# Kernel optimization log

Hardware: AMD Instinct MI355X
Metric: run time of the kernel (lower is better)

Reference implementation:

```python
import jax, jax.numpy as jnp
import numpy as np

N = 40000       # nodes
DEG = 16        # in-degree per node (self-constructed so in_deg > 0)
E = N * DEG     # edges
DIN = 128       # in_ent_feats == out_ent_feats
H = 8           # num_heads
D = DIN // H    # head_dim = 16
FF = 4 * DIN    # FFN hidden
HOPS = 5
ALPHA = 0.15
EPS = 1e-5


def _ln(x, g, b):
    m = jnp.mean(x, axis=-1, keepdims=True)
    v = jnp.mean((x - m) ** 2, axis=-1, keepdims=True)
    return (x - m) / jnp.sqrt(v + EPS) * g + b


def setup_inputs() -> dict:
    key = jax.random.key(0)
    ks = jax.random.split(key, 12)
    s = 0.05
    feat = jax.random.normal(ks[0], (N, DIN), dtype=jnp.float32)
    src = jax.random.randint(ks[1], (E,), 0, N, dtype=jnp.int32)
    # every node gets exactly DEG incoming edges -> in_degree > 0 everywhere
    dst = jnp.repeat(jnp.arange(N, dtype=jnp.int32), DEG)
    return {
        "feat": feat,
        "Wh": jax.random.normal(ks[2], (DIN, DIN), dtype=jnp.float32) * s,
        "Wt": jax.random.normal(ks[3], (DIN, DIN), dtype=jnp.float32) * s,
        "We": jax.random.normal(ks[4], (DIN, DIN), dtype=jnp.float32) * s,
        "attn_p": jax.random.normal(ks[5], (H, D), dtype=jnp.float32) * s,
        "g_head": jax.random.normal(ks[6], (H, D), dtype=jnp.float32) * s,
        "g_tail": jax.random.normal(ks[7], (H, D), dtype=jnp.float32) * s,
        "ln1_g": jnp.ones((DIN,), jnp.float32),
        "ln1_b": jnp.zeros((DIN,), jnp.float32),
        "ln2_g": jnp.ones((DIN,), jnp.float32),
        "ln2_b": jnp.zeros((DIN,), jnp.float32),
        "W1": jax.random.normal(ks[8], (FF, DIN), dtype=jnp.float32) * s,
        "b1": jnp.zeros((FF,), jnp.float32),
        "W2": jax.random.normal(ks[9], (DIN, FF), dtype=jnp.float32) * s,
        "b2": jnp.zeros((DIN,), jnp.float32),
        "src": src,
        "dst": dst,
    }


def reference(feat, Wh, Wt, We, attn_p, g_head, g_tail, ln1_g, ln1_b,
              ln2_g, ln2_b, W1, b1, W2, b2, src, dst):
    n = feat.shape[0]
    h = _ln(feat, ln1_g, ln1_b)                      # feat_drop is identity (eval)
    fh = (h @ Wh.T).reshape(n, H, D)                 # feat_head
    ft = (h @ Wt.T).reshape(n, H, D)                 # feat_tail
    fe = (h @ We.T).reshape(n, H, D)                 # feat_enti ('ft' in dgl)

    # attention logits: (u_mul_v . attn).sum(-1) / head_dim, scaled by log(in_deg) of dst
    e = jnp.sum(fh[src] * ft[dst] * attn_p, axis=-1) / D          # [E, H]
    in_deg = jax.ops.segment_sum(jnp.ones_like(dst, jnp.float32), dst, num_segments=n)
    log_in = jnp.log(in_deg)                                       # [N]
    e = e * log_in[dst][:, None]

    # gate scores
    gh = jnp.sum(fh * g_head, axis=-1)                             # [N, H]
    gt = jnp.sum(ft * g_tail, axis=-1)
    gate = jax.nn.sigmoid(gh[src] + gt[dst])                       # [E, H]

    # weighted edge softmax (per-dst stabilized, gated)
    mx = jax.ops.segment_max(e, dst, num_segments=n)               # [N, H]
    tag = jnp.exp(e - mx[dst]) * gate
    ssum = jax.ops.segment_sum(tag, dst, num_segments=n)
    a = tag / ssum[dst]                                            # [E, H]

    # PPR diffusion
    feat0 = fe
    f = feat0
    for _ in range(HOPS):
        msg = f[src] * a[..., None]                                # [E, H, D]
        agg = jax.ops.segment_sum(msg, dst, num_segments=n)
        f = (1.0 - ALPHA) * agg + ALPHA * feat0

    # residual (Identity since in == out), flatten, FFN block
    rst = (f + feat.reshape(n, H, D)).reshape(n, -1)               # [N, DIN]
    x = _ln(rst, ln2_g, ln2_b)
    ff = jax.nn.relu(x @ W1.T + b1) @ W2.T + b2
    return ff + rst
```

## Files before the change

kernel.cpp:

```cpp
#include <hip/hip_runtime.h>
#include <math.h>

#define N_NODES 40000
#define DEG 16
#define DIN 128
#define NH 8
#define DH 16
#define FFDIM 512
#define ALPHA 0.15f
#define LNEPS 1e-5f

typedef __attribute__((ext_vector_type(8))) short bf16x8;
typedef __attribute__((ext_vector_type(4))) float f32x4;
typedef __attribute__((ext_vector_type(4))) unsigned int u32x4;

__device__ inline unsigned int f2bf(float f) {
    unsigned int u = __float_as_uint(f);
    return (u + 0x7fffu + ((u >> 16) & 1u)) >> 16;
}
__device__ inline float bflo(unsigned u) { return __uint_as_float(u << 16); }
__device__ inline float bfhi(unsigned u) { return __uint_as_float(u & 0xffff0000u); }

__device__ inline float dot8(u32x4 uf, u32x4 ut, const float* __restrict__ ap) {
    float s = 0.f;
#pragma unroll
    for (int k = 0; k < 4; ++k) {
        s += bflo(uf[k]) * bflo(ut[k]) * ap[2 * k]
           + bfhi(uf[k]) * bfhi(ut[k]) * ap[2 * k + 1];
    }
    return s;
}
__device__ inline float dot8w(u32x4 u, const float* __restrict__ w) {
    float s = 0.f;
#pragma unroll
    for (int k = 0; k < 4; ++k) {
        s += bflo(u[k]) * w[2 * k] + bfhi(u[k]) * w[2 * k + 1];
    }
    return s;
}

__device__ inline float wave_sum64(float v) {
#pragma unroll
    for (int m = 32; m >= 1; m >>= 1) v += __shfl_xor(v, m, 64);
    return v;
}

__global__ void cvt_weights(const float* __restrict__ wh, const float* __restrict__ wt,
                            const float* __restrict__ we, const float* __restrict__ w1,
                            const float* __restrict__ w2,
                            short* __restrict__ owh, short* __restrict__ owt,
                            short* __restrict__ owe, short* __restrict__ ow1,
                            short* __restrict__ ow2) {
    int i = blockIdx.x * 256 + threadIdx.x;
    if (i < 16384)       owh[i]          = (short)f2bf(wh[i]);
    else if (i < 32768)  owt[i - 16384]  = (short)f2bf(wt[i - 16384]);
    else if (i < 49152)  owe[i - 32768]  = (short)f2bf(we[i - 32768]);
    else if (i < 114688) ow1[i - 49152]  = (short)f2bf(w1[i - 49152]);
    else if (i < 180224) ow2[i - 114688] = (short)f2bf(w2[i - 114688]);
}

__global__ void ln_kernel(const float* __restrict__ in, const float* __restrict__ g,
                          const float* __restrict__ b, short* __restrict__ out, int n) {
    int wid  = (blockIdx.x * blockDim.x + threadIdx.x) >> 6;
    int lane = threadIdx.x & 63;
    if (wid >= n) return;
    float2 v = *(const float2*)(in + (size_t)wid * DIN + lane * 2);
    float mean = wave_sum64(v.x + v.y) * (1.0f / DIN);
    float dx = v.x - mean, dy = v.y - mean;
    float var = wave_sum64(dx * dx + dy * dy) * (1.0f / DIN);
    float rstd = rsqrtf(var + LNEPS);
    float2 gg = *(const float2*)(g + lane * 2);
    float2 bb = *(const float2*)(b + lane * 2);
    float o0 = dx * rstd * gg.x + bb.x, o1 = dy * rstd * gg.y + bb.y;
    unsigned int pack = f2bf(o0) | (f2bf(o1) << 16);
    *(unsigned int*)(out + (size_t)wid * DIN + lane * 2) = pack;
}

__global__ void add_ln_kernel(const float* __restrict__ f, const float* __restrict__ feat,
                              const float* __restrict__ g, const float* __restrict__ b,
                              float* __restrict__ rst, short* __restrict__ x, int n) {
    int wid  = (blockIdx.x * blockDim.x + threadIdx.x) >> 6;
    int lane = threadIdx.x & 63;
    if (wid >= n) return;
    float2 va = *(const float2*)(f + (size_t)wid * DIN + lane * 2);
    float2 vb = *(const float2*)(feat + (size_t)wid * DIN + lane * 2);
    float2 r = { va.x + vb.x, va.y + vb.y };
    *(float2*)(rst + (size_t)wid * DIN + lane * 2) = r;
    float mean = wave_sum64(r.x + r.y) * (1.0f / DIN);
    float dx = r.x - mean, dy = r.y - mean;
    float var = wave_sum64(dx * dx + dy * dy) * (1.0f / DIN);
    float rstd = rsqrtf(var + LNEPS);
    float2 gg = *(const float2*)(g + lane * 2);
    float2 bb = *(const float2*)(b + lane * 2);
    float o0 = dx * rstd * gg.x + bb.x, o1 = dy * rstd * gg.y + bb.y;
    unsigned int pack = f2bf(o0) | (f2bf(o1) << 16);
    *(unsigned int*)(x + (size_t)wid * DIN + lane * 2) = pack;
}

__global__ __launch_bounds__(256) void mfma_gemm(
        const short* __restrict__ A, const short* __restrict__ B,
        int M, int N, int K,
        const float* __restrict__ bias, const float* __restrict__ res, int relu,
        float* __restrict__ Cf, short* __restrict__ Cb) {
    __shared__ __align__(16) short Al[64 * 64];
    __shared__ __align__(16) short Bl[128 * 64];
    const int t  = threadIdx.x;
    const int bm = blockIdx.x * 64;
    const int bn = blockIdx.y * 128;
    const int w = t >> 6, lane = t & 63;
    const int wr = w >> 1, wc = w & 1;
    const int l15 = lane & 15, l4 = lane >> 4;
    f32x4 acc[2][4] = {};
    for (int k0 = 0; k0 < K; k0 += 64) {
        __syncthreads();
#pragma unroll
        for (int q = 0; q < 2; ++q) {
            int c = t + q * 256;
            int r = c >> 3, kb = c & 7;
            bf16x8 v = *(const bf16x8*)(A + (size_t)(bm + r) * K + k0 + kb * 8);
            *(bf16x8*)(Al + (r * 8 + (kb ^ (r & 7))) * 8) = v;
        }
#pragma unroll
        for (int q = 0; q < 4; ++q) {
            int c = t + q * 256;
            int r = c >> 3, kb = c & 7;
            bf16x8 v = *(const bf16x8*)(B + (size_t)(bn + r) * K + k0 + kb * 8);
            *(bf16x8*)(Bl + (r * 8 + (kb ^ (r & 7))) * 8) = v;
        }
        __syncthreads();
#pragma unroll
        for (int kc = 0; kc < 2; ++kc) {
            bf16x8 af[2], bfr[4];
#pragma unroll
            for (int mf = 0; mf < 2; ++mf) {
                int row = wr * 32 + mf * 16 + l15;
                int kb = kc * 4 + l4;
                af[mf] = *(const bf16x8*)(Al + (row * 8 + (kb ^ (row & 7))) * 8);
            }
#pragma unroll
            for (int nf = 0; nf < 4; ++nf) {
                int row = wc * 64 + nf * 16 + l15;
                int kb = kc * 4 + l4;
                bfr[nf] = *(const bf16x8*)(Bl + (row * 8 + (kb ^ (row & 7))) * 8);
            }
#pragma unroll
            for (int mf = 0; mf < 2; ++mf)
#pragma unroll
                for (int nf = 0; nf < 4; ++nf)
                    acc[mf][nf] = __builtin_amdgcn_mfma_f32_16x16x32_bf16(
                        af[mf], bfr[nf], acc[mf][nf], 0, 0, 0);
        }
    }
#pragma unroll
    for (int mf = 0; mf < 2; ++mf) {
#pragma unroll
        for (int nf = 0; nf < 4; ++nf) {
            int gcol = bn + wc * 64 + nf * 16 + l15;
            float bv = bias ? bias[gcol] : 0.f;
#pragma unroll
            for (int r = 0; r < 4; ++r) {
                int grow = bm + wr * 32 + mf * 16 + l4 * 4 + r;
                float v = acc[mf][nf][r] + bv;
                if (relu) v = fmaxf(v, 0.f);
                size_t off = (size_t)grow * N + gcol;
                if (res) v += res[off];
                if (Cb) Cb[off] = (short)f2bf(v);
                if (Cf) Cf[off] = v;
            }
        }
    }
}

__global__ void attn_kernel(const short* __restrict__ fh, const short* __restrict__ ftl,
                            const float* __restrict__ g_head, const float* __restrict__ g_tail,
                            const float* __restrict__ attn_p, const int* __restrict__ src,
                            float* __restrict__ av, int n) {
    int wid  = (blockIdx.x * blockDim.x + threadIdx.x) >> 6;
    int lane = threadIdx.x & 63;
    if (wid >= n) return;
    int e  = lane & 15;
    int h0 = lane >> 4;
    int s = src[(size_t)wid * DEG + e];
    const short* fr0 = fh  + (size_t)s   * DIN + h0 * DH;
    const short* tr0 = ftl + (size_t)wid * DIN + h0 * DH;
    u32x4 f0a = *(const u32x4*)(fr0);
    u32x4 f0b = *(const u32x4*)(fr0 + 8);
    u32x4 t0a = *(const u32x4*)(tr0);
    u32x4 t0b = *(const u32x4*)(tr0 + 8);
    u32x4 f1a = *(const u32x4*)(fr0 + 64);
    u32x4 f1b = *(const u32x4*)(fr0 + 72);
    u32x4 t1a = *(const u32x4*)(tr0 + 64);
    u32x4 t1b = *(const u32x4*)(tr0 + 72);
    const float* ap0 = attn_p + h0 * DH;
    float v0 = dot8(f0a, t0a, ap0) + dot8(f0b, t0b, ap0 + 8);
    float v1 = dot8(f1a, t1a, ap0 + 64) + dot8(f1b, t1b, ap0 + 72);
    const float c = 0.17328679513998632f;
    v0 *= c; v1 *= c;
    const float* gh0 = g_head + h0 * DH;
    const float* gt0 = g_tail + h0 * DH;
    float gs0 = dot8w(f0a, gh0) + dot8w(f0b, gh0 + 8)
              + dot8w(t0a, gt0) + dot8w(t0b, gt0 + 8);
    float gs1 = dot8w(f1a, gh0 + 64) + dot8w(f1b, gh0 + 72)
              + dot8w(t1a, gt0 + 64) + dot8w(t1b, gt0 + 72);
    float m0 = v0, m1 = v1;
#pragma unroll
    for (int msk = 1; msk <= 8; msk <<= 1) {
        m0 = fmaxf(m0, __shfl_xor(m0, msk, 64));
        m1 = fmaxf(m1, __shfl_xor(m1, msk, 64));
    }
    float gate0 = 1.f / (1.f + expf(-gs0));
    float gate1 = 1.f / (1.f + expf(-gs1));
    float t0 = expf(v0 - m0) * gate0;
    float t1 = expf(v1 - m1) * gate1;
    float s0 = t0, s1 = t1;
#pragma unroll
    for (int msk = 1; msk <= 8; msk <<= 1) {
        s0 += __shfl_xor(s0, msk, 64);
        s1 += __shfl_xor(s1, msk, 64);
    }
    float* ao = av + ((size_t)wid * DEG + e) * NH;
    ao[h0]     = t0 / s0;
    ao[h0 + 4] = t1 / s1;
}

__global__ __launch_bounds__(256) void hop_kernel(
        const short* __restrict__ fin, const float* __restrict__ fe,
        const float* __restrict__ av, const int* __restrict__ src,
        short* __restrict__ fout_b, float* __restrict__ fout_f, int n) {
    __shared__ int sidx[4 * DEG];
    int wv   = threadIdx.x >> 6;
    int lane = threadIdx.x & 63;
    int wid  = blockIdx.x * 4 + wv;
    if (threadIdx.x < 4 * DEG) {
        int node = blockIdx.x * 4 + (threadIdx.x >> 4);
        sidx[threadIdx.x] = (node < n) ? src[(size_t)node * DEG + (threadIdx.x & 15)] : 0;
    }
    __syncthreads();
    if (wid >= n) return;
    int h = lane >> 3;
    const float* ae = av + (size_t)wid * DEG * NH;
    const int* se = &sidx[wv * DEG];
    float ax = 0.f, ay = 0.f;
#pragma unroll
    for (int e = 0; e < DEG; ++e) {
        int s = se[e];
        float w = ae[e * NH + h];
        unsigned u = *(const unsigned*)(fin + (size_t)s * DIN + lane * 2);
        ax += w * bflo(u);
        ay += w * bfhi(u);
    }
    float2 fev = *(const float2*)(fe + (size_t)wid * DIN + lane * 2);
    float ox = (1.f - ALPHA) * ax + ALPHA * fev.x;
    float oy = (1.f - ALPHA) * ay + ALPHA * fev.y;
    if (fout_b) {
        unsigned pack = f2bf(ox) | (f2bf(oy) << 16);
        *(unsigned*)(fout_b + (size_t)wid * DIN + lane * 2) = pack;
    } else {
        float2 o = { ox, oy };
        *(float2*)(fout_f + (size_t)wid * DIN + lane * 2) = o;
    }
}

extern "C" void kernel_launch(void* const* d_in, const int* in_sizes, int n_in,
                              void* d_out, int out_size, void* d_ws, size_t ws_size,
                              hipStream_t stream) {
    const float* feat   = (const float*)d_in[0];
    const float* Wh     = (const float*)d_in[1];
    const float* Wt     = (const float*)d_in[2];
    const float* We     = (const float*)d_in[3];
    const float* attn_p = (const float*)d_in[4];
    const float* g_head = (const float*)d_in[5];
    const float* g_tail = (const float*)d_in[6];
    const float* ln1_g  = (const float*)d_in[7];
    const float* ln1_b  = (const float*)d_in[8];
    const float* ln2_g  = (const float*)d_in[9];
    const float* ln2_b  = (const float*)d_in[10];
    const float* W1     = (const float*)d_in[11];
    const float* b1     = (const float*)d_in[12];
    const float* W2     = (const float*)d_in[13];
    const float* b2     = (const float*)d_in[14];
    const int*   src    = (const int*)d_in[15];

    float* ws = (float*)d_ws;
    float* fe   = ws;
    float* av   = ws + 5120000;
    short* h_bf   = (short*)(ws + 10880000);
    short* fh_bf  = (short*)(ws + 13440000);
    short* ftl_bf = (short*)(ws + 16000000);
    short* fe_bf  = (short*)(ws + 18560000);
    short* f0_bf  = (short*)(ws + 21120000);
    short* f1_bf  = (short*)(ws + 23680000);
    float* ffin   = ws + 26240000;
    short* x_bf   = (short*)(ws + 31360000);
    short* hidden = (short*)ws;
    short* wb     = (short*)(ws + 33920000);
    short* wh_bf = wb, *wt_bf = wb + 16384, *we_bf = wb + 32768;
    short* w1_bf = wb + 49152, *w2_bf = wb + 114688;
    float* rst = (float*)d_out;

    dim3 b256(256);
    int nodeBlocks  = (N_NODES * 64) / 256;
    int nodeBlocks4 = (N_NODES + 3) / 4;

    cvt_weights<<<704, b256, 0, stream>>>(Wh, Wt, We, W1, W2, wh_bf, wt_bf, we_bf, w1_bf, w2_bf);
    ln_kernel<<<nodeBlocks, b256, 0, stream>>>(feat, ln1_g, ln1_b, h_bf, N_NODES);

    dim3 gp(N_NODES / 64, 1);
    mfma_gemm<<<gp, b256, 0, stream>>>(h_bf, wh_bf, N_NODES, DIN, DIN, nullptr, nullptr, 0, nullptr, fh_bf);
    mfma_gemm<<<gp, b256, 0, stream>>>(h_bf, wt_bf, N_NODES, DIN, DIN, nullptr, nullptr, 0, nullptr, ftl_bf);
    mfma_gemm<<<gp, b256, 0, stream>>>(h_bf, we_bf, N_NODES, DIN, DIN, nullptr, nullptr, 0, fe, fe_bf);

    attn_kernel<<<nodeBlocks, b256, 0, stream>>>(fh_bf, ftl_bf, g_head, g_tail, attn_p, src, av, N_NODES);

    hop_kernel<<<nodeBlocks4, b256, 0, stream>>>(fe_bf, fe, av, src, f0_bf, nullptr, N_NODES);
    hop_kernel<<<nodeBlocks4, b256, 0, stream>>>(f0_bf, fe, av, src, f1_bf, nullptr, N_NODES);
    hop_kernel<<<nodeBlocks4, b256, 0, stream>>>(f1_bf, fe, av, src, f0_bf, nullptr, N_NODES);
    hop_kernel<<<nodeBlocks4, b256, 0, stream>>>(f0_bf, fe, av, src, f1_bf, nullptr, N_NODES);
    hop_kernel<<<nodeBlocks4, b256, 0, stream>>>(f1_bf, fe, av, src, nullptr, ffin, N_NODES);

    add_ln_kernel<<<nodeBlocks, b256, 0, stream>>>(ffin, feat, ln2_g, ln2_b, rst, x_bf, N_NODES);

    dim3 gff1(N_NODES / 64, FFDIM / 128);
    mfma_gemm<<<gff1, b256, 0, stream>>>(x_bf, w1_bf, N_NODES, FFDIM, DIN, b1, nullptr, 1, nullptr, hidden);
    dim3 gff2(N_NODES / 64, 1);
    mfma_gemm<<<gff2, b256, 0, stream>>>(hidden, w2_bf, N_NODES, DIN, FFDIM, b2, rst, 0, rst, nullptr);
}
```

Baseline: 373.9 us.

## Precompute per-node gate scores and widen hop gathers to 16-byte loads

Per-node gate dot products (gh, gt) are now computed once in a separate gates_kernel and read by the attention kernel, instead of being recomputed for every edge. The hop kernel is restructured so each group of 16 lanes gathers one full 256-byte source row with 16-byte vector loads, four edges at a time, and partial sums are reduced across groups with shuffles. The aim is to cut redundant arithmetic and the number of memory transactions in the gather. In exchange it adds a kernel launch, extra gather loads of gh in the attention kernel, and only one quarter of the lanes do the final writes.

```diff
diff --git a/kernel.cpp b/kernel.cpp
--- a/kernel.cpp
+++ b/kernel.cpp
@@ -27,14 +27,6 @@
     for (int k = 0; k < 4; ++k) {
         s += bflo(uf[k]) * bflo(ut[k]) * ap[2 * k]
            + bfhi(uf[k]) * bfhi(ut[k]) * ap[2 * k + 1];
-    }
-    return s;
-}
-__device__ inline float dot8w(u32x4 u, const float* __restrict__ w) {
-    float s = 0.f;
-#pragma unroll
-    for (int k = 0; k < 4; ++k) {
-        s += bflo(u[k]) * w[2 * k] + bfhi(u[k]) * w[2 * k + 1];
     }
     return s;
 }
@@ -171,8 +163,30 @@
     }
 }
 
+__global__ void gates_kernel(const short* __restrict__ fh, const short* __restrict__ ftl,
+                             const float* __restrict__ g_head, const float* __restrict__ g_tail,
+                             float* __restrict__ gh, float* __restrict__ gt, int total) {
+    int t = blockIdx.x * blockDim.x + threadIdx.x;
+    if (t >= total) return;
+    int i = t >> 3, h = t & 7;
+    const short* fp = fh + (size_t)i * DIN + h * DH;
+    const short* fq = ftl + (size_t)i * DIN + h * DH;
+    const float* gp = g_head + h * DH;
+    const float* gq = g_tail + h * DH;
+    float s1 = 0.f, s2 = 0.f;
+#pragma unroll
+    for (int d = 0; d < DH; d += 2) {
+        unsigned a = *(const unsigned*)(fp + d);
+        unsigned b = *(const unsigned*)(fq + d);
+        s1 += bflo(a) * gp[d] + bfhi(a) * gp[d + 1];
+        s2 += bflo(b) * gq[d] + bfhi(b) * gq[d + 1];
+    }
+    gh[t] = s1;
+    gt[t] = s2;
+}
+
 __global__ void attn_kernel(const short* __restrict__ fh, const short* __restrict__ ftl,
-                            const float* __restrict__ g_head, const float* __restrict__ g_tail,
+                            const float* __restrict__ ghv, const float* __restrict__ gtv,
                             const float* __restrict__ attn_p, const int* __restrict__ src,
                             float* __restrict__ av, int n) {
     int wid  = (blockIdx.x * blockDim.x + threadIdx.x) >> 6;
@@ -196,20 +210,14 @@
     float v1 = dot8(f1a, t1a, ap0 + 64) + dot8(f1b, t1b, ap0 + 72);
     const float c = 0.17328679513998632f;
     v0 *= c; v1 *= c;
-    const float* gh0 = g_head + h0 * DH;
-    const float* gt0 = g_tail + h0 * DH;
-    float gs0 = dot8w(f0a, gh0) + dot8w(f0b, gh0 + 8)
-              + dot8w(t0a, gt0) + dot8w(t0b, gt0 + 8);
-    float gs1 = dot8w(f1a, gh0 + 64) + dot8w(f1b, gh0 + 72)
-              + dot8w(t1a, gt0 + 64) + dot8w(t1b, gt0 + 72);
     float m0 = v0, m1 = v1;
 #pragma unroll
     for (int msk = 1; msk <= 8; msk <<= 1) {
         m0 = fmaxf(m0, __shfl_xor(m0, msk, 64));
         m1 = fmaxf(m1, __shfl_xor(m1, msk, 64));
     }
-    float gate0 = 1.f / (1.f + expf(-gs0));
-    float gate1 = 1.f / (1.f + expf(-gs1));
+    float gate0 = 1.f / (1.f + expf(-(ghv[(size_t)s * NH + h0]     + gtv[(size_t)wid * NH + h0])));
+    float gate1 = 1.f / (1.f + expf(-(ghv[(size_t)s * NH + h0 + 4] + gtv[(size_t)wid * NH + h0 + 4])));
     float t0 = expf(v0 - m0) * gate0;
     float t1 = expf(v1 - m1) * gate1;
     float s0 = t0, s1 = t1;
@@ -237,27 +245,46 @@
     }
     __syncthreads();
     if (wid >= n) return;
-    int h = lane >> 3;
-    const float* ae = av + (size_t)wid * DEG * NH;
-    const int* se = &sidx[wv * DEG];
-    float ax = 0.f, ay = 0.f;
-#pragma unroll
-    for (int e = 0; e < DEG; ++e) {
-        int s = se[e];
+    int grp = lane >> 4;
+    int dl  = lane & 15;
+    int h   = dl >> 1;
+    const float* ae = av + (size_t)wid * (DEG * NH);
+    float acc[8] = {};
+#pragma unroll
+    for (int it = 0; it < 4; ++it) {
+        int e = it * 4 + grp;
+        int s = sidx[wv * DEG + e];
         float w = ae[e * NH + h];
-        unsigned u = *(const unsigned*)(fin + (size_t)s * DIN + lane * 2);
-        ax += w * bflo(u);
-        ay += w * bfhi(u);
-    }
-    float2 fev = *(const float2*)(fe + (size_t)wid * DIN + lane * 2);
-    float ox = (1.f - ALPHA) * ax + ALPHA * fev.x;
-    float oy = (1.f - ALPHA) * ay + ALPHA * fev.y;
-    if (fout_b) {
-        unsigned pack = f2bf(ox) | (f2bf(oy) << 16);
-        *(unsigned*)(fout_b + (size_t)wid * DIN + lane * 2) = pack;
-    } else {
-        float2 o = { ox, oy };
-        *(float2*)(fout_f + (size_t)wid * DIN + lane * 2) = o;
+        u32x4 v = *(const u32x4*)(fin + (size_t)s * DIN + dl * 8);
+#pragma unroll
+        for (int k = 0; k < 4; ++k) {
+            acc[2 * k]     += w * bflo(v[k]);
+            acc[2 * k + 1] += w * bfhi(v[k]);
+        }
+    }
+#pragma unroll
+    for (int k = 0; k < 8; ++k) {
+        acc[k] += __shfl_xor(acc[k], 16, 64);
+        acc[k] += __shfl_xor(acc[k], 32, 64);
+    }
+    if (grp == 0) {
+        const float* fp = fe + (size_t)wid * DIN + dl * 8;
+        float o[8];
+#pragma unroll
+        for (int k = 0; k < 8; ++k)
+            o[k] = (1.f - ALPHA) * acc[k] + ALPHA * fp[k];
+        if (fout_b) {
+            unsigned pk[4];
+#pragma unroll
+            for (int k = 0; k < 4; ++k)
+                pk[k] = f2bf(o[2 * k]) | (f2bf(o[2 * k + 1]) << 16);
+            *(u32x4*)(fout_b + (size_t)wid * DIN + dl * 8) = *(u32x4*)pk;
+        } else {
+            float4 a = { o[0], o[1], o[2], o[3] };
+            float4 b = { o[4], o[5], o[6], o[7] };
+            *(float4*)(fout_f + (size_t)wid * DIN + dl * 8)     = a;
+            *(float4*)(fout_f + (size_t)wid * DIN + dl * 8 + 4) = b;
+        }
     }
 }
 
@@ -284,6 +311,8 @@
     float* ws = (float*)d_ws;
     float* fe   = ws;
     float* av   = ws + 5120000;
+    float* gh   = ws + 10240000;
+    float* gt   = ws + 10560000;
     short* h_bf   = (short*)(ws + 10880000);
     short* fh_bf  = (short*)(ws + 13440000);
     short* ftl_bf = (short*)(ws + 16000000);
@@ -310,7 +339,8 @@
     mfma_gemm<<<gp, b256, 0, stream>>>(h_bf, wt_bf, N_NODES, DIN, DIN, nullptr, nullptr, 0, nullptr, ftl_bf);
     mfma_gemm<<<gp, b256, 0, stream>>>(h_bf, we_bf, N_NODES, DIN, DIN, nullptr, nullptr, 0, fe, fe_bf);
 
-    attn_kernel<<<nodeBlocks, b256, 0, stream>>>(fh_bf, ftl_bf, g_head, g_tail, attn_p, src, av, N_NODES);
+    gates_kernel<<<(N_NODES * NH) / 256, b256, 0, stream>>>(fh_bf, ftl_bf, g_head, g_tail, gh, gt, N_NODES * NH);
+    attn_kernel<<<nodeBlocks, b256, 0, stream>>>(fh_bf, ftl_bf, gh, gt, attn_p, src, av, N_NODES);
 
     hop_kernel<<<nodeBlocks4, b256, 0, stream>>>(fe_bf, fe, av, src, f0_bf, nullptr, N_NODES);
     hop_kernel<<<nodeBlocks4, b256, 0, stream>>>(f0_bf, fe, av, src, f1_bf, nullptr, N_NODES);
```

Measured after the change: 367.7 us. No clear change (-1.7%).
